# Kernel optimization log

Measured on AMD Instinct MI355X. Metric: run time of the kernel, lower is better.

## Reference

```python
import jax, jax.numpy as jnp
import numpy as np

N, E = 10000, 160000
D, H, C, FF, L = 128, 4, 32, 512, 2
INNER = H * C
VOCAB, RELVOCAB = 32000, 100
EPS = 1e-6
GATE_BIAS = 3.0


def _layer_norm(x, w, b):
    mu = jnp.mean(x, axis=-1, keepdims=True)
    var = jnp.mean(jnp.square(x - mu), axis=-1, keepdims=True)
    return (x - mu) * jax.lax.rsqrt(var + EPS) * w + b


def setup_inputs() -> dict:
    key = jax.random.key(0)
    ks = jax.random.split(key, 24)
    s = 1.0 / np.sqrt(D)
    inp = {
        "node_ids": jax.random.randint(ks[0], (N,), 0, VOCAB),
        "edge_index": jax.random.randint(ks[1], (2, E), 0, N),
        "edge_ids": jax.random.randint(ks[2], (E,), 0, RELVOCAB),
        "node_emb": jax.random.normal(ks[3], (VOCAB, D), jnp.float32),
        "edge_emb": jax.random.normal(ks[4], (RELVOCAB, D), jnp.float32),
        # per-layer stacked params (torch Linear weight layout [out, in])
        "ln_w": jnp.ones((L, D), jnp.float32),
        "ln_b": jnp.zeros((L, D), jnp.float32),
        "q_w": jax.random.normal(ks[5], (L, INNER, D), jnp.float32) * (1.0 / np.sqrt(D * C)),
        "relA_w": jax.random.normal(ks[6], (L, FF, 2 * D), jnp.float32) * s,
        "relA_b": jnp.zeros((L, FF), jnp.float32),
        "relB_w": jax.random.normal(ks[7], (L, D, FF), jnp.float32) * s,
        "relB_b": jnp.zeros((L, D), jnp.float32),
        "relG_w": jax.random.normal(ks[8], (L, D, FF), jnp.float32) * s,
        "relG_b": jnp.zeros((L, D), jnp.float32),
        "k_w": jax.random.normal(ks[9], (L, INNER, 2 * D), jnp.float32) * s,
        "v_w": jax.random.normal(ks[10], (L, INNER, D), jnp.float32) * s,
        "o_w": jax.random.normal(ks[11], (L, D, INNER), jnp.float32) * (1.0 / np.sqrt(INNER)),
        "ff_ln_w": jnp.ones((L, D), jnp.float32),
        "ff_ln_b": jnp.zeros((L, D), jnp.float32),
        "wi_w": jax.random.normal(ks[12], (L, FF, D), jnp.float32) * s,
        "wo_w": jax.random.normal(ks[13], (L, D, FF), jnp.float32) * (1.0 / np.sqrt(FF)),
    }
    return inp


def _forward(node_ids, edge_index, edge_ids, node_emb, edge_emb, ln_w, ln_b,
             q_w, relA_w, relA_b, relB_w, relB_b, relG_w, relG_b,
             k_w, v_w, o_w, ff_ln_w, ff_ln_b, wi_w, wo_w):
    x = node_emb[node_ids]          # [N, D]
    ef = edge_emb[edge_ids]         # [E, D]
    src = edge_index[0]             # j (source / kv side)
    dst = edge_index[1]             # i (target / query side)
    for l in range(L):
        # --- relational self-attention ---
        q = _layer_norm(x, ln_w[l], ln_b[l])
        q = (q @ q_w[l].T).reshape(N, H, C)
        kv_j = x[src]                                   # [E, D]
        cat = jnp.concatenate([kv_j, ef], axis=-1)      # [E, 2D]
        inter = jax.nn.celu(cat @ relA_w[l].T + relA_b[l])   # [E, FF]
        gate = jax.nn.sigmoid(inter @ relG_w[l].T + relG_b[l] + GATE_BIAS)
        k_add = inter @ relB_w[l].T + relB_b[l]
        kv2 = kv_j * gate + k_add * (1.0 - gate)        # [E, D]
        k = (jnp.concatenate([kv2, ef], axis=-1) @ k_w[l].T).reshape(E, H, C)
        v = (kv2 @ v_w[l].T).reshape(E, H, C)
        scores = jnp.sum(q[dst] * k, axis=-1)           # [E, H]
        smax = jax.ops.segment_max(scores, dst, num_segments=N)
        ex = jnp.exp(scores - smax[dst])
        denom = jax.ops.segment_sum(ex, dst, num_segments=N)
        alpha = ex / denom[dst]                         # [E, H]
        msg = (v * alpha[..., None]).reshape(E, INNER)
        agg = jax.ops.segment_sum(msg, dst, num_segments=N)  # [N, INNER]
        x = x + agg @ o_w[l].T
        # --- feed-forward (T5-style, pre-LN, relu, residual) ---
        h = _layer_norm(x, ff_ln_w[l], ff_ln_b[l])
        x = x + jax.nn.relu(h @ wi_w[l].T) @ wo_w[l].T
    return x


def reference(node_ids, edge_index, edge_ids, node_emb, edge_emb, ln_w, ln_b,
              q_w, relA_w, relA_b, relB_w, relB_b, relG_w, relG_b,
              k_w, v_w, o_w, ff_ln_w, ff_ln_b, wi_w, wo_w):
    return _forward(node_ids, edge_index, edge_ids, node_emb, edge_emb, ln_w, ln_b,
                    q_w, relA_w, relA_b, relB_w, relB_b, relG_w, relG_b,
                    k_w, v_w, o_w, ff_ln_w, ff_ln_b, wi_w, wo_w)
```

## Files before the change

kernel.cpp:

```cpp
#include <hip/hip_runtime.h>
#include <hip/hip_bf16.h>

#define NN 10000
#define EE 160000
#define DD 128
#define HH 4
#define CC 32
#define FFF 512
#define LL 2
#define RELV 100
#define EPS 1e-6f
#define GATE_BIAS 3.0f
#define BM 32
#define NT 16

typedef __bf16 bf16x8 __attribute__((ext_vector_type(8)));
typedef float f32x4 __attribute__((ext_vector_type(4)));
typedef float f32x16 __attribute__((ext_vector_type(16)));

#define MFMA(a,b,c)   __builtin_amdgcn_mfma_f32_16x16x32_bf16((a),(b),(c),0,0,0)
#define MFMA32(a,b,c) __builtin_amdgcn_mfma_f32_32x32x16_bf16((a),(b),(c),0,0,0)

__device__ __forceinline__ int swzK(int e, int b){ return e*256 + (b ^ ((e&7)<<4)); }
__device__ __forceinline__ int swz128(int e, int b){ return e*256 + (b ^ ((e&7)<<4)); }
__device__ __forceinline__ int swz512(int e, int b){ return e*1024 + (b ^ ((e&7)<<4)); }

__global__ __launch_bounds__(256) void k_gx(
    const int* __restrict__ node_ids, const float* __restrict__ node_emb,
    float* __restrict__ x, ushort* __restrict__ xb,
    const int* __restrict__ dst, int* __restrict__ hist){
  int b = blockIdx.x, t = threadIdx.x;
  int n = b*2 + (t>>7);
  int c = t & 127;
  float v = node_emb[(long)node_ids[n]*DD + c];
  x[(long)n*DD + c] = v;
  __hip_bfloat16 h = __float2bfloat16(v);
  xb[(long)n*DD + c] = *(ushort*)&h;
  if (t < 32){
    int e = b*32 + t;
    atomicAdd(&hist[dst[e]], 1);
  }
}

__device__ __forceinline__ void wprep_one(
    const float* __restrict__ in, ushort* __restrict__ out, int tid, int IN, int instride){
  int lane = tid & 63;
  int grp  = tid >> 6;
  int nkb  = IN >> 4;
  int kb   = grp % nkb;
  int cb   = grp / nkb;
  int col  = cb*32 + (lane & 31);
  int k0   = kb*16 + (lane >> 5)*8;
  const float* p = in + (long)col*instride + k0;
  bf16x8 h;
  #pragma unroll
  for (int j=0;j<8;++j) h[j] = (__bf16)p[j];
  *(bf16x8*)(out + (long)tid*8) = h;
}

__global__ __launch_bounds__(256) void k_prep2(
    const float* __restrict__ relG_w, const float* __restrict__ relB_w,
    const float* __restrict__ k_w, const float* __restrict__ v_w,
    const float* __restrict__ relA_w,
    const float* __restrict__ q_w, const float* __restrict__ o_w,
    const float* __restrict__ wi_w, const float* __restrict__ wo_w,
    ushort* __restrict__ Gwb, ushort* __restrict__ Bwb,
    ushort* __restrict__ Kwb, ushort* __restrict__ Vwb, ushort* __restrict__ A1b,
    ushort* __restrict__ Qwb, ushort* __restrict__ Owb,
    ushort* __restrict__ Wib, ushort* __restrict__ Wob){
  const int bid = blockIdx.x;
  const int l   = bid >> 8;
  const int tidl = (bid & 255)*256 + threadIdx.x;
  const long gid = (long)bid*256 + threadIdx.x;
  if (tidl < DD*FFF/8){
    wprep_one(relG_w + (long)l*DD*FFF, Gwb + (long)l*DD*FFF, tidl, FFF, FFF);
    wprep_one(relB_w + (long)l*DD*FFF, Bwb + (long)l*DD*FFF, tidl, FFF, FFF);
  }
  if (tidl < DD*DD/8){
    wprep_one(k_w + (long)l*DD*256, Kwb + (long)l*DD*DD, tidl, DD, 256);
    wprep_one(v_w + (long)l*DD*DD,  Vwb + (long)l*DD*DD, tidl, DD, DD);
  }
  {
    int o = tidl / DD, i = tidl % DD;
    __hip_bfloat16 h = __float2bfloat16(relA_w[(long)l*FFF*256 + (long)o*256 + i]);
    A1b[(long)l*FFF*DD + tidl] = *(ushort*)&h;
  }
  if (gid < (long)LL*DD*DD){
    __hip_bfloat16 h1 = __float2bfloat16(q_w[gid]); Qwb[gid] = *(ushort*)&h1;
    __hip_bfloat16 h2 = __float2bfloat16(o_w[gid]); Owb[gid] = *(ushort*)&h2;
  }
  {
    __hip_bfloat16 h3 = __float2bfloat16(wi_w[gid]); Wib[gid] = *(ushort*)&h3;
    __hip_bfloat16 h4 = __float2bfloat16(wo_w[gid]); Wob[gid] = *(ushort*)&h4;
  }
}

__global__ __launch_bounds__(256) void k_ea2(
    const float* __restrict__ edge_emb, const float* __restrict__ relA_w,
    const float* __restrict__ relA_b, const float* __restrict__ k_w,
    ushort* __restrict__ EA2b, float* __restrict__ EKf){
  int l = blockIdx.x / RELV, rel = blockIdx.x % RELV, t = threadIdx.x;
  const float* Aw = relA_w + (long)l*FFF*256;
  const float* Ab = relA_b + (long)l*FFF;
  const float* Kw = k_w + (long)l*DD*256;
  ushort* EAo = EA2b + (long)l*RELV*FFF;
  float* EKo  = EKf + (long)l*RELV*DD;
  __shared__ float emb[128];
  if (t < 128) emb[t] = edge_emb[(long)rel*DD + t];
  __syncthreads();
  for (int f=t; f<FFF; f+=256){
    const float* wr = Aw + (long)f*256 + 128;
    float s = Ab[f];
    for (int i=0;i<128;++i) s += emb[i]*wr[i];
    __hip_bfloat16 h = __float2bfloat16(s);
    EAo[(long)rel*FFF + f] = *(ushort*)&h;
  }
  if (t < 128){
    const float* wr = Kw + (long)t*256 + 128;
    float s = 0.f;
    for (int i=0;i<128;++i) s += emb[i]*wr[i];
    EKo[(long)rel*DD + t] = s;
  }
}

__global__ __launch_bounds__(256) void k_scan(const int* __restrict__ hist, int* __restrict__ cursor){
  __shared__ int tsum[256];
  const int t = threadIdx.x;
  const int PER = (NN + 255) / 256;
  const int base = t*PER;
  int s = 0;
  for (int i=0;i<PER;++i){ int idx = base+i; if (idx < NN) s += hist[idx]; }
  tsum[t] = s;
  __syncthreads();
  if (t == 0){
    int run = 0;
    for (int i=0;i<256;++i){ int v = tsum[i]; tsum[i] = run; run += v; }
  }
  __syncthreads();
  int run = tsum[t];
  for (int i=0;i<PER;++i){
    int idx = base+i;
    if (idx < NN){ int v = hist[idx]; cursor[idx] = run; run += v; }
  }
}
__global__ __launch_bounds__(256) void k_scatter(const int* __restrict__ dst,
    int* __restrict__ cursor, int* __restrict__ perm){
  int e = blockIdx.x*256 + threadIdx.x;
  if (e < EE){
    int p = atomicAdd(&cursor[dst[e]], 1);
    perm[p] = e;
  }
}

__global__ __launch_bounds__(256) void k_lnq_xa(
    const float* __restrict__ x, const float* __restrict__ lnw, const float* __restrict__ lnb,
    const ushort* __restrict__ qwb, const ushort* __restrict__ a1b,
    float* __restrict__ q, ushort* __restrict__ XAb,
    float* __restrict__ agg, float* __restrict__ denom){
  __shared__ __align__(16) unsigned char HB[NT*256];
  __shared__ __align__(16) unsigned char HR[NT*256];
  const int n0 = blockIdx.x*NT;
  const int t = threadIdx.x;
  const int e = t>>4, s = t&15;
  const int w = t>>6, l = t&63, lr = l&15, lg = l>>4;
  {
    float4 z4 = {0.f,0.f,0.f,0.f};
    float* ap = agg + (long)n0*DD + t*8;
    *(float4*)ap = z4; *(float4*)(ap+4) = z4;
    if (t < NT*HH) denom[n0*HH + t] = 0.f;
  }
  {
    const float* xp = x + (long)(n0+e)*DD + s*8;
    float xv[8];
    *(float4*)&xv[0] = *(const float4*)xp;
    *(float4*)&xv[4] = *(const float4*)(xp+4);
    float sm = 0.f;
    #pragma unroll
    for (int i=0;i<8;++i) sm += xv[i];
    sm += __shfl_xor(sm,1); sm += __shfl_xor(sm,2);
    sm += __shfl_xor(sm,4); sm += __shfl_xor(sm,8);
    float mu = sm*(1.f/DD);
    float sq = 0.f;
    #pragma unroll
    for (int i=0;i<8;++i){ float d = xv[i]-mu; sq += d*d; }
    sq += __shfl_xor(sq,1); sq += __shfl_xor(sq,2);
    sq += __shfl_xor(sq,4); sq += __shfl_xor(sq,8);
    float rstd = rsqrtf(sq*(1.f/DD) + EPS);
    float4 w0 = *(const float4*)(lnw + s*8), w1 = *(const float4*)(lnw + s*8 + 4);
    float4 b0 = *(const float4*)(lnb + s*8), b1 = *(const float4*)(lnb + s*8 + 4);
    float wv[8] = {w0.x,w0.y,w0.z,w0.w,w1.x,w1.y,w1.z,w1.w};
    float bv[8] = {b0.x,b0.y,b0.z,b0.w,b1.x,b1.y,b1.z,b1.w};
    bf16x8 hb, hr;
    #pragma unroll
    for (int i=0;i<8;++i){
      hb[i] = (__bf16)((xv[i]-mu)*rstd*wv[i] + bv[i]);
      hr[i] = (__bf16)xv[i];
    }
    *(bf16x8*)(HB + swz128(e, s*16)) = hb;
    *(bf16x8*)(HR + swz128(e, s*16)) = hr;
  }
  __syncthreads();
  {
    const int o0 = w*32;
    f32x4 z = {0.f,0.f,0.f,0.f};
    f32x4 acc[2] = {z,z};
    #pragma unroll
    for (int k4=0;k4<4;++k4){
      bf16x8 a = *(const bf16x8*)(HB + swz128(lr, k4*64 + lg*16));
      #pragma unroll
      for (int nt=0;nt<2;++nt){
        bf16x8 b = *(const bf16x8*)(qwb + (long)(o0+nt*16+lr)*128 + k4*32 + lg*8);
        acc[nt] = MFMA(a, b, acc[nt]);
      }
    }
    #pragma unroll
    for (int nt=0;nt<2;++nt)
      #pragma unroll
      for (int r=0;r<4;++r)
        q[(long)(n0 + lg*4 + r)*DD + o0 + nt*16 + lr] = acc[nt][r];
  }
  {
    const int f0w = w*128;
    f32x4 z = {0.f,0.f,0.f,0.f};
    f32x4 acc[8] = {z,z,z,z,z,z,z,z};
    #pragma unroll
    for (int k4=0;k4<4;++k4){
      bf16x8 a = *(const bf16x8*)(HR + swz128(lr, k4*64 + lg*16));
      #pragma unroll
      for (int nt=0;nt<8;++nt){
        bf16x8 b = *(const bf16x8*)(a1b + (long)(f0w+nt*16+lr)*128 + k4*32 + lg*8);
        acc[nt] = MFMA(a, b, acc[nt]);
      }
    }
    #pragma unroll
    for (int nt=0;nt<8;++nt)
      #pragma unroll
      for (int r=0;r<4;++r){
        __hip_bfloat16 h = __float2bfloat16(acc[nt][r]);
        XAb[(long)(n0+lg*4+r)*FFF + f0w+nt*16+lr] = *(ushort*)&h;
      }
  }
}

__global__ __launch_bounds__(256,4) void k_edge(
    const ushort* __restrict__ xb, const ushort* __restrict__ XAb,
    const ushort* __restrict__ EAb, const float* __restrict__ EKf,
    const float* __restrict__ q,
    const int* __restrict__ src, const int* __restrict__ dst, const int* __restrict__ eids,
    const int* __restrict__ perm,
    const ushort* __restrict__ Gwb, const float* __restrict__ Gb,
    const ushort* __restrict__ Bwb, const float* __restrict__ Bb,
    const ushort* __restrict__ Kwb, const ushort* __restrict__ Vwb,
    float* __restrict__ agg, float* __restrict__ denom)
{
  __shared__ __align__(16) unsigned char KVB[BM*256];
  __shared__ __align__(16) unsigned char INTB[2][BM*256];
  __shared__ int srcl[BM], dstl[BM], eidl[BM];

  int nb;
  {
    const int cpx = (EE/BM) >> 3;
    nb = (blockIdx.x & 7)*cpx + (blockIdx.x >> 3);
  }
  const int e0 = nb * BM;
  const int t  = threadIdx.x;
  const int w  = t >> 6;
  const int l  = t & 63;
  const int c32 = l & 31;
  const int hi  = l >> 5;
  const int C = w;
  const int oc = C*32 + c32;

  if (t < BM){
    int pe = perm[e0+t];
    srcl[t] = src[pe]; dstl[t] = dst[pe]; eidl[t] = eids[pe];
  }
  __syncthreads();

  {
    const uint4* xbu = (const uint4*)xb;
    #pragma unroll
    for (int it=0; it<2; ++it){
      int g = it*256 + t;
      int e = g >> 4, qq = g & 15;
      *(uint4*)(KVB + swzK(e, qq*16)) = xbu[(long)srcl[e]*16 + qq];
    }
  }

  f32x16 gbG, gbB;
  {
    float bg = Gb[oc] + GATE_BIAS;
    float bb = Bb[oc];
    #pragma unroll
    for (int i=0;i<16;++i){ gbG[i] = bg; gbB[i] = bb; }
  }

  bf16x8 xa8[2], ea8[2];
  #pragma unroll
  for (int it=0; it<2; ++it){
    int g = it*256 + t;
    int e = g >> 4, c8 = g & 15;
    xa8[it] = *(const bf16x8*)(XAb + (long)srcl[e]*FFF + c8*8);
    ea8[it] = *(const bf16x8*)(EAb + (long)eidl[e]*FFF + c8*8);
  }

  #pragma unroll
  for (int ch=0; ch<4; ++ch){
    bf16x8 o[2];
    #pragma unroll
    for (int it=0; it<2; ++it){
      #pragma unroll
      for (int j=0;j<8;++j){
        float s = (float)xa8[it][j] + (float)ea8[it][j];
        o[it][j] = (__bf16)((s > 0.f) ? s : (__expf(s) - 1.f));
      }
    }
    unsigned char* INTp = INTB[ch & 1];
    #pragma unroll
    for (int it=0; it<2; ++it){
      int g = it*256 + t;
      int e = g >> 4, c8 = g & 15;
      *(bf16x8*)(INTp + swzK(e, c8*16)) = o[it];
    }
    __syncthreads();
    if (ch < 3){
      #pragma unroll
      for (int it=0; it<2; ++it){
        int g = it*256 + t;
        int e = g >> 4, c8 = g & 15;
        xa8[it] = *(const bf16x8*)(XAb + (long)srcl[e]*FFF + (ch+1)*128 + c8*8);
        ea8[it] = *(const bf16x8*)(EAb + (long)eidl[e]*FFF + (ch+1)*128 + c8*8);
      }
    }
    {
      const ushort* Wg = Gwb + ((long)(C*32 + ch*8)*64 + l)*8;
      bf16x8 wf[8];
      #pragma unroll
      for (int i=0;i<8;++i) wf[i] = *(const bf16x8*)(Wg + (long)i*512);
      #pragma unroll
      for (int i=0;i<8;++i){
        bf16x8 a = *(const bf16x8*)(INTp + swzK(c32, i*32 + hi*16));
        gbG = MFMA32(a, wf[i], gbG);
      }
    }
    {
      const ushort* Wb = Bwb + ((long)(C*32 + ch*8)*64 + l)*8;
      bf16x8 wf[8];
      #pragma unroll
      for (int i=0;i<8;++i) wf[i] = *(const bf16x8*)(Wb + (long)i*512);
      #pragma unroll
      for (int i=0;i<8;++i){
        bf16x8 a = *(const bf16x8*)(INTp + swzK(c32, i*32 + hi*16));
        gbB = MFMA32(a, wf[i], gbB);
      }
    }
  }

  #pragma unroll
  for (int r=0;r<16;++r){
    int row = (r&3) + 8*(r>>2) + 4*hi;
    float g  = 1.f/(1.f + __expf(-gbG[r]));
    float kv = (float)*(const __bf16*)(KVB + swzK(row, oc*2));
    float k2 = gbB[r] + g*(kv - gbB[r]);
    *(__bf16*)(KVB + swzK(row, oc*2)) = (__bf16)k2;
  }
  __syncthreads();

  f32x16 ka, va;
  #pragma unroll
  for (int i=0;i<16;++i){ ka[i] = 0.f; va[i] = 0.f; }
  {
    const ushort* Wk = Kwb + ((long)(C*8)*64 + l)*8;
    bf16x8 wf[8];
    #pragma unroll
    for (int i=0;i<8;++i) wf[i] = *(const bf16x8*)(Wk + (long)i*512);
    #pragma unroll
    for (int i=0;i<8;++i){
      bf16x8 a = *(const bf16x8*)(KVB + swzK(c32, i*32 + hi*16));
      ka = MFMA32(a, wf[i], ka);
    }
  }
  {
    const ushort* Wv = Vwb + ((long)(C*8)*64 + l)*8;
    bf16x8 wf[8];
    #pragma unroll
    for (int i=0;i<8;++i) wf[i] = *(const bf16x8*)(Wv + (long)i*512);
    #pragma unroll
    for (int i=0;i<8;++i){
      bf16x8 a = *(const bf16x8*)(KVB + swzK(c32, i*32 + hi*16));
      va = MFMA32(a, wf[i], va);
    }
  }

  #pragma unroll
  for (int qq=0; qq<4; ++qq){
    const int base = 8*qq + 4*hi;
    float ex[4];
    #pragma unroll
    for (int j=0;j<4;++j){
      int r = qq*4 + j;
      int gr = base + j;
      float kv = ka[r] + EKf[(long)eidl[gr]*DD + oc];
      float p = kv * q[(long)dstl[gr]*DD + oc];
      p += __shfl_xor(p, 1); p += __shfl_xor(p, 2);
      p += __shfl_xor(p, 4); p += __shfl_xor(p, 8);
      p += __shfl_xor(p, 16);
      ex[j] = __expf(p);
    }
    {
      float acc = va[qq*4]*ex[0];
      int cur = dstl[base];
      #pragma unroll
      for (int j=1;j<4;++j){
        int dn = dstl[base+j];
        if (dn != cur){
          atomicAdd(&agg[(long)cur*DD + oc], acc);
          acc = 0.f; cur = dn;
        }
        acc += va[qq*4+j]*ex[j];
      }
      atomicAdd(&agg[(long)cur*DD + oc], acc);
    }
    if (c32 == 0){
      float da = ex[0];
      int cur = dstl[base];
      #pragma unroll
      for (int j=1;j<4;++j){
        int dn = dstl[base+j];
        if (dn != cur){
          atomicAdd(&denom[cur*HH + C], da);
          da = 0.f; cur = dn;
        }
        da += ex[j];
      }
      atomicAdd(&denom[cur*HH + C], da);
    }
  }
}

template<bool FUSE_LNQ>
__global__ __launch_bounds__(256) void k_node(
    const float* __restrict__ agg, const float* __restrict__ denom,
    const ushort* __restrict__ owb,
    const float* __restrict__ lnw, const float* __restrict__ lnb,
    const ushort* __restrict__ wib, const ushort* __restrict__ wob,
    float* __restrict__ x, ushort* __restrict__ xb,
    const float* __restrict__ nlnw, const float* __restrict__ nlnb,
    const ushort* __restrict__ nqwb, const ushort* __restrict__ na1b,
    float* __restrict__ q, ushort* __restrict__ XAb){
  __shared__ __align__(16) unsigned char AB[NT*256];
  __shared__ __align__(16) unsigned char IB[NT*1024];
  __shared__ __align__(16) float XO[NT][132];
  const int n0 = blockIdx.x*NT;
  const int t = threadIdx.x;
  const int e = t>>4, s = t&15;
  const int w = t>>6, l = t&63, lr = l&15, lg = l>>4;

  {
    const float* ap = agg + (long)(n0+e)*DD + s*8;
    float av[8];
    *(float4*)&av[0] = *(const float4*)ap;
    *(float4*)&av[4] = *(const float4*)(ap+4);
    float dinv = 1.f / denom[(n0+e)*HH + (s>>2)];
    bf16x8 hb;
    #pragma unroll
    for (int i=0;i<8;++i) hb[i] = (__bf16)(av[i]*dinv);
    *(bf16x8*)(AB + swz128(e, s*16)) = hb;
  }
  __syncthreads();

  {
    const int o0 = w*32;
    f32x4 z = {0.f,0.f,0.f,0.f};
    f32x4 acc[2] = {z,z};
    #pragma unroll
    for (int k4=0;k4<4;++k4){
      bf16x8 a = *(const bf16x8*)(AB + swz128(lr, k4*64 + lg*16));
      #pragma unroll
      for (int nt=0;nt<2;++nt){
        bf16x8 b = *(const bf16x8*)(owb + (long)(o0+nt*16+lr)*128 + k4*32 + lg*8);
        acc[nt] = MFMA(a, b, acc[nt]);
      }
    }
    #pragma unroll
    for (int nt=0;nt<2;++nt)
      #pragma unroll
      for (int r=0;r<4;++r)
        XO[lg*4+r][o0+nt*16+lr] = acc[nt][r];
  }
  __syncthreads();

  float x1[8];
  {
    const float* xp = x + (long)(n0+e)*DD + s*8;
    float xv[8];
    *(float4*)&xv[0] = *(const float4*)xp;
    *(float4*)&xv[4] = *(const float4*)(xp+4);
    #pragma unroll
    for (int i=0;i<8;++i) x1[i] = xv[i] + XO[e][s*8+i];
    float sm = 0.f;
    #pragma unroll
    for (int i=0;i<8;++i) sm += x1[i];
    sm += __shfl_xor(sm,1); sm += __shfl_xor(sm,2);
    sm += __shfl_xor(sm,4); sm += __shfl_xor(sm,8);
    float mu = sm*(1.f/DD);
    float sq = 0.f;
    #pragma unroll
    for (int i=0;i<8;++i){ float d = x1[i]-mu; sq += d*d; }
    sq += __shfl_xor(sq,1); sq += __shfl_xor(sq,2);
    sq += __shfl_xor(sq,4); sq += __shfl_xor(sq,8);
    float rstd = rsqrtf(sq*(1.f/DD) + EPS);
    float4 w0 = *(const float4*)(lnw + s*8), w1 = *(const float4*)(lnw + s*8 + 4);
    float4 b0 = *(const float4*)(lnb + s*8), b1 = *(const float4*)(lnb + s*8 + 4);
    float wv[8] = {w0.x,w0.y,w0.z,w0.w,w1.x,w1.y,w1.z,w1.w};
    float bv[8] = {b0.x,b0.y,b0.z,b0.w,b1.x,b1.y,b1.z,b1.w};
    bf16x8 hb;
    #pragma unroll
    for (int i=0;i<8;++i) hb[i] = (__bf16)((x1[i]-mu)*rstd*wv[i] + bv[i]);
    __syncthreads();
    *(bf16x8*)(AB + swz128(e, s*16)) = hb;
  }
  __syncthreads();

  {
    const int f0w = w*128;
    f32x4 z = {0.f,0.f,0.f,0.f};
    f32x4 acc[8] = {z,z,z,z,z,z,z,z};
    #pragma unroll
    for (int k4=0;k4<4;++k4){
      bf16x8 a = *(const bf16x8*)(AB + swz128(lr, k4*64 + lg*16));
      #pragma unroll
      for (int nt=0;nt<8;++nt){
        bf16x8 b = *(const bf16x8*)(wib + (long)(f0w+nt*16+lr)*128 + k4*32 + lg*8);
        acc[nt] = MFMA(a, b, acc[nt]);
      }
    }
    #pragma unroll
    for (int nt=0;nt<8;++nt)
      #pragma unroll
      for (int r=0;r<4;++r){
        int e2 = lg*4 + r;
        int f = f0w + nt*16 + lr;
        float va = acc[nt][r];
        *(__bf16*)(IB + swz512(e2, f*2)) = (__bf16)fmaxf(va, 0.f);
      }
  }
  __syncthreads();

  {
    const int o0 = w*32;
    f32x4 z = {0.f,0.f,0.f,0.f};
    f32x4 acc[2] = {z,z};
    #pragma unroll
    for (int k16=0;k16<16;++k16){
      bf16x8 a = *(const bf16x8*)(IB + swz512(lr, k16*64 + lg*16));
      #pragma unroll
      for (int nt=0;nt<2;++nt){
        bf16x8 b = *(const bf16x8*)(wob + (long)(o0+nt*16+lr)*512 + k16*32 + lg*8);
        acc[nt] = MFMA(a, b, acc[nt]);
      }
    }
    #pragma unroll
    for (int nt=0;nt<2;++nt)
      #pragma unroll
      for (int r=0;r<4;++r)
        XO[lg*4+r][o0+nt*16+lr] = acc[nt][r];
  }
  __syncthreads();

  float xn[8];
  {
    #pragma unroll
    for (int i=0;i<8;++i) xn[i] = x1[i] + XO[e][s*8+i];
    float* xp = x + (long)(n0+e)*DD + s*8;
    *(float4*)xp = *(float4*)&xn[0];
    *(float4*)(xp+4) = *(float4*)&xn[4];
    bf16x8 hb;
    #pragma unroll
    for (int i=0;i<8;++i) hb[i] = (__bf16)xn[i];
    *(bf16x8*)(xb + (long)(n0+e)*DD + s*8) = hb;
  }

  if constexpr (FUSE_LNQ){
    {
      float4 z4 = {0.f,0.f,0.f,0.f};
      float* ap = (float*)agg + (long)n0*DD + t*8;
      *(float4*)ap = z4; *(float4*)(ap+4) = z4;
      if (t < NT*HH) ((float*)denom)[n0*HH + t] = 0.f;
    }
    {
      float sm = 0.f;
      #pragma unroll
      for (int i=0;i<8;++i) sm += xn[i];
      sm += __shfl_xor(sm,1); sm += __shfl_xor(sm,2);
      sm += __shfl_xor(sm,4); sm += __shfl_xor(sm,8);
      float mu = sm*(1.f/DD);
      float sq = 0.f;
      #pragma unroll
      for (int i=0;i<8;++i){ float d = xn[i]-mu; sq += d*d; }
      sq += __shfl_xor(sq,1); sq += __shfl_xor(sq,2);
      sq += __shfl_xor(sq,4); sq += __shfl_xor(sq,8);
      float rstd = rsqrtf(sq*(1.f/DD) + EPS);
      float4 w0 = *(const float4*)(nlnw + s*8), w1 = *(const float4*)(nlnw + s*8 + 4);
      float4 b0 = *(const float4*)(nlnb + s*8), b1 = *(const float4*)(nlnb + s*8 + 4);
      float wv[8] = {w0.x,w0.y,w0.z,w0.w,w1.x,w1.y,w1.z,w1.w};
      float bv[8] = {b0.x,b0.y,b0.z,b0.w,b1.x,b1.y,b1.z,b1.w};
      bf16x8 hb, hr;
      #pragma unroll
      for (int i=0;i<8;++i){
        hb[i] = (__bf16)((xn[i]-mu)*rstd*wv[i] + bv[i]);
        hr[i] = (__bf16)xn[i];
      }
      *(bf16x8*)(AB + swz128(e, s*16)) = hb;
      *(bf16x8*)(IB + swz128(e, s*16)) = hr;
    }
    __syncthreads();
    {
      const int o0 = w*32;
      f32x4 z = {0.f,0.f,0.f,0.f};
      f32x4 acc[2] = {z,z};
      #pragma unroll
      for (int k4=0;k4<4;++k4){
        bf16x8 a = *(const bf16x8*)(AB + swz128(lr, k4*64 + lg*16));
        #pragma unroll
        for (int nt=0;nt<2;++nt){
          bf16x8 b = *(const bf16x8*)(nqwb + (long)(o0+nt*16+lr)*128 + k4*32 + lg*8);
          acc[nt] = MFMA(a, b, acc[nt]);
        }
      }
      #pragma unroll
      for (int nt=0;nt<2;++nt)
        #pragma unroll
        for (int r=0;r<4;++r)
          q[(long)(n0 + lg*4 + r)*DD + o0 + nt*16 + lr] = acc[nt][r];
    }
    {
      const int f0w = w*128;
      f32x4 z = {0.f,0.f,0.f,0.f};
      f32x4 acc[8] = {z,z,z,z,z,z,z,z};
      #pragma unroll
      for (int k4=0;k4<4;++k4){
        bf16x8 a = *(const bf16x8*)(IB + swz128(lr, k4*64 + lg*16));
        #pragma unroll
        for (int nt=0;nt<8;++nt){
          bf16x8 b = *(const bf16x8*)(na1b + (long)(f0w+nt*16+lr)*128 + k4*32 + lg*8);
          acc[nt] = MFMA(a, b, acc[nt]);
        }
      }
      #pragma unroll
      for (int nt=0;nt<8;++nt)
        #pragma unroll
        for (int r=0;r<4;++r){
          __hip_bfloat16 h = __float2bfloat16(acc[nt][r]);
          XAb[(long)(n0+lg*4+r)*FFF + f0w+nt*16+lr] = *(ushort*)&h;
        }
    }
  }
}

extern "C" void kernel_launch(void* const* d_in, const int* in_sizes, int n_in,
                              void* d_out, int out_size, void* d_ws, size_t ws_size,
                              hipStream_t stream) {
  const int* node_ids   = (const int*)d_in[0];
  const int* edge_index = (const int*)d_in[1];
  const int* edge_ids   = (const int*)d_in[2];
  const float* node_emb = (const float*)d_in[3];
  const float* edge_emb = (const float*)d_in[4];
  const float* ln_w   = (const float*)d_in[5];
  const float* ln_b   = (const float*)d_in[6];
  const float* q_w    = (const float*)d_in[7];
  const float* relA_w = (const float*)d_in[8];
  const float* relA_b = (const float*)d_in[9];
  const float* relB_w = (const float*)d_in[10];
  const float* relB_b = (const float*)d_in[11];
  const float* relG_w = (const float*)d_in[12];
  const float* relG_b = (const float*)d_in[13];
  const float* k_w    = (const float*)d_in[14];
  const float* v_w    = (const float*)d_in[15];
  const float* o_w    = (const float*)d_in[16];
  const float* ff_ln_w= (const float*)d_in[17];
  const float* ff_ln_b= (const float*)d_in[18];
  const float* wi_w   = (const float*)d_in[19];
  const float* wo_w   = (const float*)d_in[20];
  const int* src = edge_index;
  const int* dst = edge_index + EE;

  float* ws = (float*)d_ws;
  float* x   = ws;  ws += (long)NN*DD;
  float* q   = ws;  ws += (long)NN*DD;
  float* denom = ws; ws += NN*HH;
  float* agg   = ws; ws += (long)NN*DD;
  float* EKf   = ws; ws += (long)LL*RELV*DD;
  int* hist   = (int*)ws; ws += NN;
  int* perm   = (int*)ws; ws += EE;
  ushort* xb  = (ushort*)ws; ws += (long)NN*DD/2;
  ushort* XAb = (ushort*)ws; ws += (long)NN*FFF/2;
  ushort* EAb = (ushort*)ws; ws += (long)LL*RELV*FFF/2;
  ushort* A1b = (ushort*)ws; ws += (long)LL*FFF*DD/2;
  ushort* Gwb = (ushort*)ws; ws += (long)LL*DD*FFF/2;
  ushort* Bwb = (ushort*)ws; ws += (long)LL*DD*FFF/2;
  ushort* Kwb = (ushort*)ws; ws += (long)LL*DD*DD/2;
  ushort* Vwb = (ushort*)ws; ws += (long)LL*DD*DD/2;
  ushort* Qwb = (ushort*)ws; ws += (long)LL*DD*DD/2;
  ushort* Owb = (ushort*)ws; ws += (long)LL*DD*DD/2;
  ushort* Wib = (ushort*)ws; ws += (long)LL*FFF*DD/2;
  ushort* Wob = (ushort*)ws; ws += (long)LL*DD*FFF/2;

  hipMemsetAsync(hist, 0, NN*sizeof(int), stream);
  k_gx<<<NN/2, 256, 0, stream>>>(node_ids, node_emb, x, xb, dst, hist);
  k_scan<<<1, 256, 0, stream>>>(hist, hist);
  k_scatter<<<(EE+255)/256, 256, 0, stream>>>(dst, hist, perm);
  k_prep2<<<512, 256, 0, stream>>>(relG_w, relB_w, k_w, v_w, relA_w,
                                   q_w, o_w, wi_w, wo_w,
                                   Gwb, Bwb, Kwb, Vwb, A1b, Qwb, Owb, Wib, Wob);
  k_ea2<<<2*RELV, 256, 0, stream>>>(edge_emb, relA_w, relA_b, k_w, EAb, EKf);

  k_lnq_xa<<<NN/NT, 256, 0, stream>>>(x, ln_w, ln_b, Qwb, A1b, q, XAb, agg, denom);
  for (int l=0; l<LL; ++l){
    k_edge<<<EE/BM, 256, 0, stream>>>(xb, XAb, EAb + (long)l*RELV*FFF, EKf + (long)l*RELV*DD,
        q, src, dst, edge_ids, perm,
        Gwb + (long)l*DD*FFF,  relG_b + (long)l*DD,
        Bwb + (long)l*DD*FFF,  relB_b + (long)l*DD,
        Kwb + (long)l*DD*DD,   Vwb + (long)l*DD*DD,
        agg, denom);
    if (l < LL-1){
      k_node<true><<<NN/NT, 256, 0, stream>>>(agg, denom, Owb + (long)l*DD*DD,
          ff_ln_w + l*DD, ff_ln_b + l*DD,
          Wib + (long)l*FFF*DD, Wob + (long)l*DD*FFF, x, xb,
          ln_w + (l+1)*DD, ln_b + (l+1)*DD,
          Qwb + (long)(l+1)*DD*DD, A1b + (long)(l+1)*FFF*DD, q, XAb);
    } else {
      k_node<false><<<NN/NT, 256, 0, stream>>>(agg, denom, Owb + (long)l*DD*DD,
          ff_ln_w + l*DD, ff_ln_b + l*DD,
          Wib + (long)l*FFF*DD, Wob + (long)l*DD*FFF, x, xb,
          nullptr, nullptr, nullptr, nullptr, nullptr, nullptr);
    }
  }
  hipMemcpyAsync(d_out, x, (size_t)NN*DD*sizeof(float), hipMemcpyDeviceToDevice, stream);
}
```

Measured before the change: 411.3 us.

## Fuse embedding gather into front kernel, warp-scan prefix, write final output directly

Removes the separate gather kernel by folding the node-embedding lookup, x/xb writes and the destination histogram into the LN+Q kernel, which now runs before scan and scatter. Replaces the serial single-thread prefix in the scan with a wave shuffle scan. The last node kernel writes straight to the output buffer, which drops the trailing device-to-device copy and skips an unneeded bf16 store. This cuts launches and memory traffic, at the cost of histogram atomics inside the front kernel.

```diff
diff --git a/kernel.cpp b/kernel.cpp
--- a/kernel.cpp
+++ b/kernel.cpp
@@ -24,23 +24,6 @@
 __device__ __forceinline__ int swzK(int e, int b){ return e*256 + (b ^ ((e&7)<<4)); }
 __device__ __forceinline__ int swz128(int e, int b){ return e*256 + (b ^ ((e&7)<<4)); }
 __device__ __forceinline__ int swz512(int e, int b){ return e*1024 + (b ^ ((e&7)<<4)); }
-
-__global__ __launch_bounds__(256) void k_gx(
-    const int* __restrict__ node_ids, const float* __restrict__ node_emb,
-    float* __restrict__ x, ushort* __restrict__ xb,
-    const int* __restrict__ dst, int* __restrict__ hist){
-  int b = blockIdx.x, t = threadIdx.x;
-  int n = b*2 + (t>>7);
-  int c = t & 127;
-  float v = node_emb[(long)node_ids[n]*DD + c];
-  x[(long)n*DD + c] = v;
-  __hip_bfloat16 h = __float2bfloat16(v);
-  xb[(long)n*DD + c] = *(ushort*)&h;
-  if (t < 32){
-    int e = b*32 + t;
-    atomicAdd(&hist[dst[e]], 1);
-  }
-}
 
 __device__ __forceinline__ void wprep_one(
     const float* __restrict__ in, ushort* __restrict__ out, int tid, int IN, int instride){
@@ -124,20 +107,26 @@
 }
 
 __global__ __launch_bounds__(256) void k_scan(const int* __restrict__ hist, int* __restrict__ cursor){
-  __shared__ int tsum[256];
+  __shared__ int wsum[4];
   const int t = threadIdx.x;
   const int PER = (NN + 255) / 256;
   const int base = t*PER;
   int s = 0;
   for (int i=0;i<PER;++i){ int idx = base+i; if (idx < NN) s += hist[idx]; }
-  tsum[t] = s;
-  __syncthreads();
-  if (t == 0){
-    int run = 0;
-    for (int i=0;i<256;++i){ int v = tsum[i]; tsum[i] = run; run += v; }
-  }
-  __syncthreads();
-  int run = tsum[t];
+  int inc = s;
+  #pragma unroll
+  for (int off=1; off<64; off<<=1){
+    int v = __shfl_up(inc, off);
+    if ((t & 63) >= off) inc += v;
+  }
+  if ((t & 63) == 63) wsum[t >> 6] = inc;
+  __syncthreads();
+  int woff = 0;
+  {
+    int w = t >> 6;
+    for (int i=0;i<w;++i) woff += wsum[i];
+  }
+  int run = woff + inc - s;
   for (int i=0;i<PER;++i){
     int idx = base+i;
     if (idx < NN){ int v = hist[idx]; cursor[idx] = run; run += v; }
@@ -152,9 +141,12 @@
   }
 }
 
-__global__ __launch_bounds__(256) void k_lnq_xa(
-    const float* __restrict__ x, const float* __restrict__ lnw, const float* __restrict__ lnb,
+__global__ __launch_bounds__(256) void k_front(
+    const int* __restrict__ node_ids, const float* __restrict__ node_emb,
+    const int* __restrict__ dst, int* __restrict__ hist,
+    const float* __restrict__ lnw, const float* __restrict__ lnb,
     const ushort* __restrict__ qwb, const ushort* __restrict__ a1b,
+    float* __restrict__ x, ushort* __restrict__ xb,
     float* __restrict__ q, ushort* __restrict__ XAb,
     float* __restrict__ agg, float* __restrict__ denom){
   __shared__ __align__(16) unsigned char HB[NT*256];
@@ -164,16 +156,25 @@
   const int e = t>>4, s = t&15;
   const int w = t>>6, l = t&63, lr = l&15, lg = l>>4;
   {
+    int eg = blockIdx.x*256 + t;
+    atomicAdd(&hist[dst[eg]], 1);
+  }
+  {
     float4 z4 = {0.f,0.f,0.f,0.f};
     float* ap = agg + (long)n0*DD + t*8;
     *(float4*)ap = z4; *(float4*)(ap+4) = z4;
     if (t < NT*HH) denom[n0*HH + t] = 0.f;
   }
   {
-    const float* xp = x + (long)(n0+e)*DD + s*8;
+    const float* xp = node_emb + (long)node_ids[n0+e]*DD + s*8;
     float xv[8];
     *(float4*)&xv[0] = *(const float4*)xp;
     *(float4*)&xv[4] = *(const float4*)(xp+4);
+    {
+      float* xo = x + (long)(n0+e)*DD + s*8;
+      *(float4*)xo = *(float4*)&xv[0];
+      *(float4*)(xo+4) = *(float4*)&xv[4];
+    }
     float sm = 0.f;
     #pragma unroll
     for (int i=0;i<8;++i) sm += xv[i];
@@ -198,6 +199,7 @@
     }
     *(bf16x8*)(HB + swz128(e, s*16)) = hb;
     *(bf16x8*)(HR + swz128(e, s*16)) = hr;
+    *(bf16x8*)(xb + (long)(n0+e)*DD + s*8) = hr;
   }
   __syncthreads();
   {
@@ -444,7 +446,7 @@
     const ushort* __restrict__ owb,
     const float* __restrict__ lnw, const float* __restrict__ lnb,
     const ushort* __restrict__ wib, const ushort* __restrict__ wob,
-    float* __restrict__ x, ushort* __restrict__ xb,
+    float* __restrict__ x, ushort* __restrict__ xb, float* __restrict__ xout,
     const float* __restrict__ nlnw, const float* __restrict__ nlnb,
     const ushort* __restrict__ nqwb, const ushort* __restrict__ na1b,
     float* __restrict__ q, ushort* __restrict__ XAb){
@@ -569,19 +571,23 @@
   __syncthreads();
 
   float xn[8];
-  {
-    #pragma unroll
-    for (int i=0;i<8;++i) xn[i] = x1[i] + XO[e][s*8+i];
-    float* xp = x + (long)(n0+e)*DD + s*8;
+  #pragma unroll
+  for (int i=0;i<8;++i) xn[i] = x1[i] + XO[e][s*8+i];
+
+  if constexpr (!FUSE_LNQ){
+    float* xp = xout + (long)(n0+e)*DD + s*8;
     *(float4*)xp = *(float4*)&xn[0];
     *(float4*)(xp+4) = *(float4*)&xn[4];
-    bf16x8 hb;
-    #pragma unroll
-    for (int i=0;i<8;++i) hb[i] = (__bf16)xn[i];
-    *(bf16x8*)(xb + (long)(n0+e)*DD + s*8) = hb;
-  }
-
-  if constexpr (FUSE_LNQ){
+  } else {
+    {
+      float* xp = x + (long)(n0+e)*DD + s*8;
+      *(float4*)xp = *(float4*)&xn[0];
+      *(float4*)(xp+4) = *(float4*)&xn[4];
+      bf16x8 hb;
+      #pragma unroll
+      for (int i=0;i<8;++i) hb[i] = (__bf16)xn[i];
+      *(bf16x8*)(xb + (long)(n0+e)*DD + s*8) = hb;
+    }
     {
       float4 z4 = {0.f,0.f,0.f,0.f};
       float* ap = (float*)agg + (long)n0*DD + t*8;
@@ -707,15 +713,15 @@
   ushort* Wob = (ushort*)ws; ws += (long)LL*DD*FFF/2;
 
   hipMemsetAsync(hist, 0, NN*sizeof(int), stream);
-  k_gx<<<NN/2, 256, 0, stream>>>(node_ids, node_emb, x, xb, dst, hist);
-  k_scan<<<1, 256, 0, stream>>>(hist, hist);
-  k_scatter<<<(EE+255)/256, 256, 0, stream>>>(dst, hist, perm);
   k_prep2<<<512, 256, 0, stream>>>(relG_w, relB_w, k_w, v_w, relA_w,
                                    q_w, o_w, wi_w, wo_w,
                                    Gwb, Bwb, Kwb, Vwb, A1b, Qwb, Owb, Wib, Wob);
   k_ea2<<<2*RELV, 256, 0, stream>>>(edge_emb, relA_w, relA_b, k_w, EAb, EKf);
-
-  k_lnq_xa<<<NN/NT, 256, 0, stream>>>(x, ln_w, ln_b, Qwb, A1b, q, XAb, agg, denom);
+  k_front<<<NN/NT, 256, 0, stream>>>(node_ids, node_emb, dst, hist,
+      ln_w, ln_b, Qwb, A1b, x, xb, q, XAb, agg, denom);
+  k_scan<<<1, 256, 0, stream>>>(hist, hist);
+  k_scatter<<<(EE+255)/256, 256, 0, stream>>>(dst, hist, perm);
+
   for (int l=0; l<LL; ++l){
     k_edge<<<EE/BM, 256, 0, stream>>>(xb, XAb, EAb + (long)l*RELV*FFF, EKf + (long)l*RELV*DD,
         q, src, dst, edge_ids, perm,
@@ -726,15 +732,14 @@
     if (l < LL-1){
       k_node<true><<<NN/NT, 256, 0, stream>>>(agg, denom, Owb + (long)l*DD*DD,
           ff_ln_w + l*DD, ff_ln_b + l*DD,
-          Wib + (long)l*FFF*DD, Wob + (long)l*DD*FFF, x, xb,
+          Wib + (long)l*FFF*DD, Wob + (long)l*DD*FFF, x, xb, x,
           ln_w + (l+1)*DD, ln_b + (l+1)*DD,
           Qwb + (long)(l+1)*DD*DD, A1b + (long)(l+1)*FFF*DD, q, XAb);
     } else {
       k_node<false><<<NN/NT, 256, 0, stream>>>(agg, denom, Owb + (long)l*DD*DD,
           ff_ln_w + l*DD, ff_ln_b + l*DD,
-          Wib + (long)l*FFF*DD, Wob + (long)l*DD*FFF, x, xb,
+          Wib + (long)l*FFF*DD, Wob + (long)l*DD*FFF, x, xb, (float*)d_out,
           nullptr, nullptr, nullptr, nullptr, nullptr, nullptr);
     }
   }
-  hipMemcpyAsync(d_out, x, (size_t)NN*DD*sizeof(float), hipMemcpyDeviceToDevice, stream);
-}
+}
```

New measurement: 403.2 us (median of 2 runs). 1.02x faster.
